# Performance work log

Hardware: AMD Instinct MI355X
Metric: run time of the kernel (lower is better)

## Reference

```python
import jax, jax.numpy as jnp
import numpy as np

B, S, E, H = 2, 2048, 2048, 8
D = E // H          # 256, also PMSNorm width
LAYER_IDX = 3
EPS = 1e-5
NEG = jnp.finfo(jnp.float32).min


def setup_inputs() -> dict:
    key = jax.random.key(0)
    k1, k2, k3 = jax.random.split(key, 3)
    return {
        "hidden_state": jax.random.normal(k1, (B, S, E), dtype=jnp.float32),
        "w_attn": jax.random.normal(k2, (E, 3 * E), dtype=jnp.float32) * 0.02,
        "w_proj": jax.random.normal(k3, (E, E), dtype=jnp.float32) * 0.02,
        "norm_weight": jnp.ones((D,), dtype=jnp.float32),
    }


def reference(hidden_state, w_attn, w_proj, norm_weight):
    # qkv projection (Linear, no bias): [B,S,3E]
    qkv = hidden_state @ w_attn
    q, k, v = jnp.split(qkv, 3, axis=-1)
    # split heads -> [B,H,S,D]
    q = q.reshape(B, S, H, D).transpose(0, 2, 1, 3)
    k = k.reshape(B, S, H, D).transpose(0, 2, 1, 3)
    v = v.reshape(B, S, H, D).transpose(0, 2, 1, 3)
    # scaled scores, extra layer-idx scaling as in the module
    scale = jnp.asarray(D, jnp.float32) ** 0.5 * (LAYER_IDX + 1)
    scores = jnp.einsum("bhqd,bhkd->bhqk", q, k) / scale
    # causal mask (tril buffer): masked positions -> float32 min
    causal = jnp.tril(jnp.ones((S, S), dtype=bool))
    scores = jnp.where(causal[None, None], scores, NEG)
    attn = jax.nn.softmax(scores, axis=-1)  # dropout is identity in eval
    o = jnp.einsum("bhqk,bhkd->bhqd", attn, v)
    # PMSNorm over last dim D (applied per-head, as in the source)
    o = o * jax.lax.rsqrt(jnp.mean(o * o, axis=-1, keepdims=True) + EPS)
    o = o * norm_weight
    # merge heads -> [B,S,E], output projection
    merged = o.transpose(0, 2, 1, 3).reshape(B, S, E)
    return merged @ w_proj
```

## Files before the change

kernel.cpp:

```cpp
#include <hip/hip_runtime.h>
#include <math.h>


typedef unsigned short u16;
typedef unsigned int   u32;
typedef u16   u16x8 __attribute__((ext_vector_type(8)));
typedef __bf16 bf16x8 __attribute__((ext_vector_type(8)));
typedef float f32x4 __attribute__((ext_vector_type(4)));

#define GPTR(p) ((const __attribute__((address_space(1))) void*)(p))
#define LPTR(p) ((__attribute__((address_space(3))) void*)(p))

__device__ __forceinline__ u16 f2bf(float x) {
  u32 u = __float_as_uint(x);
  return (u16)((u + 0x7fffu + ((u >> 16) & 1u)) >> 16);
}

__device__ __forceinline__ bf16x8 ld8(const void* p) {
  u16x8 v = *reinterpret_cast<const u16x8*>(p);
  return __builtin_bit_cast(bf16x8, v);
}

__device__ __forceinline__ void g2l16(const void* g, void* l) {
  __builtin_amdgcn_global_load_lds(GPTR(g), LPTR(l), 16, 0, 0);
}

__global__ void prep_kernel(const float* __restrict__ hs, const float* __restrict__ wat,
                            const float* __restrict__ wpr, u16* __restrict__ Xb,
                            u16* __restrict__ Wa_t, u16* __restrict__ Wp_t) {
  __shared__ float t[32][33];
  const int bid = blockIdx.x, tid = threadIdx.x;
  if (bid < 4096) {
    int i = bid * 256 + tid;
    const float4* p = reinterpret_cast<const float4*>(hs) + (size_t)i * 2;
    float4 a = p[0], b = p[1];
    u16x8 v;
    v[0] = f2bf(a.x); v[1] = f2bf(a.y); v[2] = f2bf(a.z); v[3] = f2bf(a.w);
    v[4] = f2bf(b.x); v[5] = f2bf(b.y); v[6] = f2bf(b.z); v[7] = f2bf(b.w);
    reinterpret_cast<u16x8*>(Xb)[i] = v;
    return;
  }
  const float* in; u16* out; int R, C, bx, by;
  if (bid < 16384) {
    int b2 = bid - 4096;
    in = wat; out = Wa_t; R = 2048; C = 6144;
    bx = (b2 % 192) * 32; by = (b2 / 192) * 32;
  } else {
    int b3 = bid - 16384;
    in = wpr; out = Wp_t; R = 2048; C = 2048;
    bx = (b3 % 64) * 32; by = (b3 / 64) * 32;
  }
  int x = tid & 31, y = tid >> 5;
  #pragma unroll
  for (int k = 0; k < 32; k += 8)
    t[y + k][x] = in[(size_t)(by + y + k) * C + (bx + x)];
  __syncthreads();
  #pragma unroll
  for (int k = 0; k < 32; k += 8)
    out[(size_t)(bx + y + k) * R + (by + x)] = f2bf(t[x][y + k]);
}

__global__ void tv_kernel(const u16* __restrict__ qkv, u16* __restrict__ out) {
  __shared__ u16 t[32][33];
  int bh = blockIdx.z, b = bh >> 3, h = bh & 7;
  const u16* ip = qkv + (size_t)b * 2048 * 6144 + 4096 + h * 256;
  u16* op = out + (size_t)bh * 256 * 2048;
  int bx = blockIdx.x * 32, by = blockIdx.y * 32;
  int x = threadIdx.x, y = threadIdx.y;
  #pragma unroll
  for (int k = 0; k < 32; k += 8)
    t[y + k][x] = ip[(size_t)(by + y + k) * 6144 + (bx + x)];
  __syncthreads();
  #pragma unroll
  for (int k = 0; k < 32; k += 8)
    op[(size_t)(bx + y + k) * 2048 + (by + x)] = t[x][y + k];
}

template<int WM, int WN, int MF, int NF, bool F32OUT>
__global__ __launch_bounds__(512, 4) void gemm2b_kernel(
    const u16* __restrict__ A, const u16* __restrict__ Bt,
    float* __restrict__ Cf, u16* __restrict__ Cb, int M, int N, int K) {
  constexpr int BM = WM * MF * 16;
  constexpr int BN = WN * NF * 16;
  constexpr int TILEB = (BM + BN) * 128;
  constexpr int NSTG = TILEB / 8192;
  __shared__ __align__(16) char smem[2 * TILEB];

  const int tid = threadIdx.x, lane = tid & 63, w = tid >> 6;
  const int wr = w / WN, wc = w % WN;
  const int g = lane >> 4, li = lane & 15;
  const int bn = blockIdx.x * BN, bm = blockIdx.y * BM;

  const char* src[NSTG]; u32 dOff[NSTG];
  #pragma unroll
  for (int j = 0; j < NSTG; ++j) {
    int o = j * 8192 + tid * 16;
    if (o < BM * 128) {
      int row = o >> 7;
      int col = (o & 127) ^ ((row & 7) << 4);
      src[j] = (const char*)A + (size_t)(bm + row) * K * 2 + col;
    } else {
      int rem = o - BM * 128;
      int row = rem >> 7;
      int col = (rem & 127) ^ ((row & 7) << 4);
      src[j] = (const char*)Bt + (size_t)(bn + row) * K * 2 + col;
    }
    dOff[j] = (u32)(o - lane * 16);
  }

  u32 aRd[2][MF], bRd[2][NF];
  #pragma unroll
  for (int ks = 0; ks < 2; ++ks) {
    #pragma unroll
    for (int mf = 0; mf < MF; ++mf) {
      int row = wr * (MF * 16) + mf * 16 + li;
      aRd[ks][mf] = row * 128 + ((ks * 64 + g * 16) ^ ((row & 7) << 4));
    }
    #pragma unroll
    for (int nf = 0; nf < NF; ++nf) {
      int row = wc * (NF * 16) + nf * 16 + li;
      bRd[ks][nf] = BM * 128 + row * 128 + ((ks * 64 + g * 16) ^ ((row & 7) << 4));
    }
  }

  const f32x4 fz = {0.f, 0.f, 0.f, 0.f};
  f32x4 acc[MF][NF];
  #pragma unroll
  for (int i = 0; i < MF; ++i)
    #pragma unroll
    for (int j = 0; j < NF; ++j) acc[i][j] = fz;

  const int NT = K >> 6;
  #pragma unroll
  for (int j = 0; j < NSTG; ++j) { g2l16(src[j], smem + dOff[j]); src[j] += 128; }

  for (int t = 0; t < NT; ++t) {
    const int cur = t & 1;
    const bool more = (t + 1 < NT);
    asm volatile("s_barrier" ::: "memory");
    if (more) {
      char* nb = smem + (cur ^ 1) * TILEB;
      #pragma unroll
      for (int j = 0; j < NSTG; ++j) { g2l16(src[j], nb + dOff[j]); src[j] += 128; }
      asm volatile("s_waitcnt vmcnt(%0)" :: "i"(NSTG) : "memory");
    } else {
      asm volatile("s_waitcnt vmcnt(0)" ::: "memory");
    }
    asm volatile("s_barrier" ::: "memory");

    const char* sb = smem + cur * TILEB;
    #pragma unroll
    for (int ks = 0; ks < 2; ++ks) {
      bf16x8 aR[MF], bR[NF];
      #pragma unroll
      for (int mf = 0; mf < MF; ++mf) aR[mf] = ld8(sb + aRd[ks][mf]);
      #pragma unroll
      for (int nf = 0; nf < NF; ++nf) bR[nf] = ld8(sb + bRd[ks][nf]);
      __builtin_amdgcn_s_setprio(1);
      #pragma unroll
      for (int mf = 0; mf < MF; ++mf)
        #pragma unroll
        for (int nf = 0; nf < NF; ++nf)
          acc[mf][nf] = __builtin_amdgcn_mfma_f32_16x16x32_bf16(aR[mf], bR[nf], acc[mf][nf], 0, 0, 0);
      __builtin_amdgcn_s_setprio(0);
    }
  }

  #pragma unroll
  for (int mf = 0; mf < MF; ++mf)
    #pragma unroll
    for (int nf = 0; nf < NF; ++nf)
      #pragma unroll
      for (int r = 0; r < 4; ++r) {
        int gm = bm + wr * (MF * 16) + mf * 16 + g * 4 + r;
        int gn = bn + wc * (NF * 16) + nf * 16 + li;
        if (F32OUT) Cf[(size_t)gm * N + gn] = acc[mf][nf][r];
        else        Cb[(size_t)gm * N + gn] = f2bf(acc[mf][nf][r]);
      }
}

__global__ __launch_bounds__(512, 2) void attn_kernel(
    const u16* __restrict__ qkv, const u16* __restrict__ Vt,
    const float* __restrict__ nw, u16* __restrict__ Mrg) {
  __shared__ __align__(16) char smem[106496];
  char* sKb = smem;
  char* sVb = smem + 65536;
  char* sPb = smem + 65536 + 32768;
  float* oex  = (float*)smem;
  float* mlex = (float*)(smem + 65536);

  const int c = blockIdx.x;
  const int bh = c & 15, iu = c >> 4;
  const int b = bh >> 3, h = bh & 7;
  const int tid = threadIdx.x, lane = tid & 63, w = tid >> 6;
  const int kh = w >> 2, wq = w & 3;
  const int g = lane >> 4, li = lane & 15;
  const float MASKV = -30000.0f;
  const float MINIT = -1000.0f;
  const float isc = 1.0f / 64.0f;
  const f32x4 fz = {0.f, 0.f, 0.f, 0.f};
  const size_t KADV = (size_t)32 * 6144 * 2;

  #pragma unroll 1
  for (int uu = 0; uu < 2; ++uu) {
    const int qt = uu ? (31 - iu) : iu;
    const int nt = qt + 1;
    const int kvb0 = kh * nt * 32;

    int qrow = qt * 64 + wq * 16 + li;
    const u16* qp = qkv + (size_t)(b * 2048 + qrow) * 6144 + h * 256;
    bf16x8 qf[8];
    #pragma unroll
    for (int c8 = 0; c8 < 8; ++c8) qf[c8] = ld8(qp + c8 * 32 + g * 8);

    const char* kSrc[4]; u32 kDoff[4];
    #pragma unroll
    for (int j = 0; j < 4; ++j) {
      int chunk = wq * 4 + j;
      int o = chunk * 1024 + lane * 16;
      int row = o >> 9, cb = o & 511;
      int cbs = cb ^ ((row & 7) << 4);
      kSrc[j] = (const char*)qkv + ((size_t)(b * 2048 + kvb0 + row) * 6144 + 2048 + h * 256) * 2 + cbs;
      kDoff[j] = chunk * 1024;
    }
    const char* vSrc[4]; char* vDst[4];
    #pragma unroll
    for (int j = 0; j < 4; ++j) {
      int chunk = wq * 4 + j;
      int o = chunk * 1024 + lane * 16;
      int row = o >> 6, cb = o & 63;
      int cbs = cb ^ (((row >> 1) & 3) << 4);
      vSrc[j] = (const char*)Vt + ((size_t)(bh * 256 + row) * 2048 + kvb0) * 2 + cbs;
      vDst[j] = sVb + kh * 16384 + chunk * 1024;
    }

    f32x4 o_[16];
    #pragma unroll
    for (int nf = 0; nf < 16; ++nf) o_[nf] = fz;
    float m_[4] = {MINIT, MINIT, MINIT, MINIT};
    float l_[4] = {0.f, 0.f, 0.f, 0.f};

    {
      char* kb0 = sKb + (kh * 2 + 0) * 16384;
      #pragma unroll
      for (int j = 0; j < 4; ++j) { g2l16(kSrc[j], kb0 + kDoff[j]); kSrc[j] += KADV; }
    }
    asm volatile("s_waitcnt vmcnt(0)" ::: "memory");
    asm volatile("s_barrier" ::: "memory");

    int cur = 0;
    for (int t = 0; t < nt; ++t) {
      const bool more = (t < nt - 1);
      #pragma unroll
      for (int j = 0; j < 4; ++j) { g2l16(vSrc[j], vDst[j]); vSrc[j] += 64; }
      if (more) {
        char* kb = sKb + (kh * 2 + (cur ^ 1)) * 16384;
        #pragma unroll
        for (int j = 0; j < 4; ++j) { g2l16(kSrc[j], kb + kDoff[j]); kSrc[j] += KADV; }
      }

      f32x4 sacc[2];
      const char* kbase = sKb + (kh * 2 + cur) * 16384;
      __builtin_amdgcn_s_setprio(1);
      #pragma unroll
      for (int nf = 0; nf < 2; ++nf) {
        int row = nf * 16 + li;
        int swz = (row & 7) << 4;
        const char* kr = kbase + row * 512;
        f32x4 sa = fz, sb = fz;
        #pragma unroll
        for (int c8 = 0; c8 < 4; ++c8) {
          sa = __builtin_amdgcn_mfma_f32_16x16x32_bf16(qf[c8],     ld8(kr + ((c8 * 64 + g * 16) ^ swz)),       sa, 0, 0, 0);
          sb = __builtin_amdgcn_mfma_f32_16x16x32_bf16(qf[c8 + 4], ld8(kr + (((c8 + 4) * 64 + g * 16) ^ swz)), sb, 0, 0, 0);
        }
        sacc[nf] = sa + sb;
      }
      __builtin_amdgcn_s_setprio(0);

      const int tidx = kh * nt + t;
      const bool diag = (tidx >= 2 * qt);
      float p[2][4], m0[4];
      #pragma unroll
      for (int r = 0; r < 4; ++r) {
        int qr = qt * 64 + wq * 16 + g * 4 + r;
        float a0 = sacc[0][r] * isc;
        float a1 = sacc[1][r] * isc;
        if (diag) {
          if (tidx * 32 + li > qr) a0 = MASKV;
          if (tidx * 32 + 16 + li > qr) a1 = MASKV;
        }
        p[0][r] = a0; p[1][r] = a1;
        m0[r] = fmaxf(a0, a1);
      }
      bool need = (m0[0] > m_[0] + 8.f) || (m0[1] > m_[1] + 8.f) ||
                  (m0[2] > m_[2] + 8.f) || (m0[3] > m_[3] + 8.f);
      if (__any(need)) {
        #pragma unroll
        for (int r = 0; r < 4; ++r) {
          float mx = m0[r];
          mx = fmaxf(mx, __shfl_xor(mx, 1));
          mx = fmaxf(mx, __shfl_xor(mx, 2));
          mx = fmaxf(mx, __shfl_xor(mx, 4));
          mx = fmaxf(mx, __shfl_xor(mx, 8));
          float mn = fmaxf(m_[r], mx);
          float sc = __expf(m_[r] - mn);
          l_[r] *= sc; m_[r] = mn;
          #pragma unroll
          for (int nf = 0; nf < 16; ++nf) o_[nf][r] *= sc;
        }
      }
      #pragma unroll
      for (int r = 0; r < 4; ++r) {
        float e0 = __expf(p[0][r] - m_[r]);
        float e1 = __expf(p[1][r] - m_[r]);
        p[0][r] = e0; p[1][r] = e1;
        l_[r] += e0 + e1;
      }

      if (more) asm volatile("s_waitcnt vmcnt(4)" ::: "memory");
      else      asm volatile("s_waitcnt vmcnt(0)" ::: "memory");
      asm volatile("s_barrier" ::: "memory");

      char* sPw = sPb + kh * 4096 + wq * 1024;
      #pragma unroll
      for (int r = 0; r < 4; ++r) {
        int row = g * 4 + r;
        int swz = ((row >> 1) & 3) << 4;
        #pragma unroll
        for (int nf = 0; nf < 2; ++nf)
          *(u16*)(sPw + row * 64 + (((nf * 16 + li) * 2) ^ swz)) = f2bf(p[nf][r]);
      }
      asm volatile("s_waitcnt lgkmcnt(0)" ::: "memory");
      __builtin_amdgcn_sched_barrier(0);

      __builtin_amdgcn_s_setprio(1);
      {
        const char* vb = sVb + kh * 16384;
        bf16x8 pa = ld8(sPw + li * 64 + ((g * 16) ^ (((li >> 1) & 3) << 4)));
        #pragma unroll
        for (int nf = 0; nf < 16; ++nf) {
          int row = nf * 16 + li;
          bf16x8 vf = ld8(vb + row * 64 + ((g * 16) ^ (((row >> 1) & 3) << 4)));
          o_[nf] = __builtin_amdgcn_mfma_f32_16x16x32_bf16(pa, vf, o_[nf], 0, 0, 0);
        }
      }
      __builtin_amdgcn_s_setprio(0);

      asm volatile("s_barrier" ::: "memory");
      if (more) asm volatile("s_waitcnt vmcnt(0)" ::: "memory");
      cur ^= 1;
    }

    if (kh == 1) {
      #pragma unroll
      for (int nf = 0; nf < 16; ++nf)
        *(f32x4*)(oex + wq * 4096 + nf * 256 + lane * 4) = o_[nf];
      #pragma unroll
      for (int r = 0; r < 4; ++r) {
        mlex[wq * 512 + r * 64 + lane] = l_[r];
        mlex[wq * 512 + 256 + r * 64 + lane] = m_[r];
      }
    }
    __syncthreads();
    if (kh == 0) {
      float aw[4], bw[4], inv_l[4];
      #pragma unroll
      for (int r = 0; r < 4; ++r) {
        float mB = mlex[wq * 512 + 256 + r * 64 + lane];
        float lB = mlex[wq * 512 + r * 64 + lane];
        float mm = fmaxf(m_[r], mB);
        aw[r] = __expf(m_[r] - mm);
        bw[r] = __expf(mB - mm);
        float lr = l_[r] * aw[r] + lB * bw[r];
        lr += __shfl_xor(lr, 1);
        lr += __shfl_xor(lr, 2);
        lr += __shfl_xor(lr, 4);
        lr += __shfl_xor(lr, 8);
        inv_l[r] = 1.0f / lr;
      }
      #pragma unroll
      for (int nf = 0; nf < 16; ++nf) {
        f32x4 ob = *(f32x4*)(oex + wq * 4096 + nf * 256 + lane * 4);
        #pragma unroll
        for (int r = 0; r < 4; ++r)
          o_[nf][r] = o_[nf][r] * aw[r] + ob[r] * bw[r];
      }
      #pragma unroll
      for (int r = 0; r < 4; ++r) {
        float ss = 0.f;
        #pragma unroll
        for (int nf = 0; nf < 16; ++nf) {
          float v = o_[nf][r] * inv_l[r];
          ss += v * v;
        }
        ss += __shfl_xor(ss, 1);
        ss += __shfl_xor(ss, 2);
        ss += __shfl_xor(ss, 4);
        ss += __shfl_xor(ss, 8);
        float rms = rsqrtf(ss * (1.0f / 256.0f) + 1e-5f);
        int row = qt * 64 + wq * 16 + g * 4 + r;
        #pragma unroll
        for (int nf = 0; nf < 16; ++nf) {
          int d = nf * 16 + li;
          float v = o_[nf][r] * inv_l[r] * rms * nw[d];
          Mrg[((size_t)(b * 2048 + row)) * 2048 + h * 256 + d] = f2bf(v);
        }
      }
    }
    __syncthreads();
  }
}

extern "C" void kernel_launch(void* const* d_in, const int* in_sizes, int n_in,
                              void* d_out, int out_size, void* d_ws, size_t ws_size,
                              hipStream_t stream) {
  const float* hs  = (const float*)d_in[0];
  const float* wat = (const float*)d_in[1];
  const float* wpr = (const float*)d_in[2];
  const float* nw  = (const float*)d_in[3];
  float* out = (float*)d_out;

  char* ws = (char*)d_ws;
  u16* Xb   = (u16*)(ws + 0);
  u16* Wp_t = (u16*)(ws + (16u << 20));
  u16* Qkv  = (u16*)(ws + (24u << 20));
  u16* Vt   = (u16*)(ws + (72u << 20));
  u16* Mrg  = Xb;
  u16* Wa_t = (u16*)d_out;

  dim3 t328(32, 8);
  prep_kernel<<<20480, 256, 0, stream>>>(hs, wat, wpr, Xb, Wa_t, Wp_t);
  gemm2b_kernel<2, 4, 4, 3, false><<<dim3(32, 32), 512, 0, stream>>>(
      Xb, Wa_t, nullptr, Qkv, 4096, 6144, 2048);
  tv_kernel<<<dim3(8, 64, 16), t328, 0, stream>>>(Qkv, Vt);
  attn_kernel<<<256, 512, 0, stream>>>(Qkv, Vt, nw, Mrg);
  gemm2b_kernel<2, 4, 4, 2, true><<<dim3(16, 32), 512, 0, stream>>>(
      Mrg, Wp_t, out, nullptr, 4096, 2048, 2048);
  (void)in_sizes; (void)n_in; (void)out_size; (void)ws_size;
}
```

Measured before the change: 233.1 us.

## Split attention KV halves into separate blocks with a merge kernel

The in-block split-K attention, where two warp groups each handled half of the KV range and merged through shared memory, becomes a split-KV scheme across separate 256-thread blocks. Each block writes a normalized bf16 partial output and its log-sum-exp to global memory. A new merge kernel combines the two partials and applies the RMS norm. This doubles the grid and cuts shared memory per block, which should improve occupancy and scheduling, at the cost of an extra launch, a global round trip for the partials, and bf16 rounding of the partial outputs.

```diff
diff --git a/kernel.cpp b/kernel.cpp
--- a/kernel.cpp
+++ b/kernel.cpp
@@ -14,6 +14,10 @@
 __device__ __forceinline__ u16 f2bf(float x) {
   u32 u = __float_as_uint(x);
   return (u16)((u + 0x7fffu + ((u >> 16) & 1u)) >> 16);
+}
+
+__device__ __forceinline__ float bf2f(u16 x) {
+  return __uint_as_float(((u32)x) << 16);
 }
 
 __device__ __forceinline__ bf16x8 ld8(const void* p) {
@@ -179,21 +183,17 @@
       }
 }
 
-__global__ __launch_bounds__(512, 2) void attn_kernel(
+__global__ __launch_bounds__(256, 2) void attn_main_kernel(
     const u16* __restrict__ qkv, const u16* __restrict__ Vt,
-    const float* __restrict__ nw, u16* __restrict__ Mrg) {
-  __shared__ __align__(16) char smem[106496];
-  char* sKb = smem;
-  char* sVb = smem + 65536;
-  char* sPb = smem + 65536 + 32768;
-  float* oex  = (float*)smem;
-  float* mlex = (float*)(smem + 65536);
+    u16* __restrict__ Opart, float* __restrict__ Lse) {
+  __shared__ __align__(16) u16 sK[2][32 * 256];
+  __shared__ __align__(16) u16 sV[256 * 32];
+  __shared__ __align__(16) u16 sP[4 * 16 * 32];
 
   const int c = blockIdx.x;
-  const int bh = c & 15, iu = c >> 4;
+  const int bh = c & 15, iu = (c >> 4) & 15, half = c >> 8;
   const int b = bh >> 3, h = bh & 7;
-  const int tid = threadIdx.x, lane = tid & 63, w = tid >> 6;
-  const int kh = w >> 2, wq = w & 3;
+  const int tid = threadIdx.x, lane = tid & 63, wq = tid >> 6;
   const int g = lane >> 4, li = lane & 15;
   const float MASKV = -30000.0f;
   const float MINIT = -1000.0f;
@@ -205,7 +205,7 @@
   for (int uu = 0; uu < 2; ++uu) {
     const int qt = uu ? (31 - iu) : iu;
     const int nt = qt + 1;
-    const int kvb0 = kh * nt * 32;
+    const int kvb0 = half * nt * 32;
 
     int qrow = qt * 64 + wq * 16 + li;
     const u16* qp = qkv + (size_t)(b * 2048 + qrow) * 6144 + h * 256;
@@ -231,7 +231,7 @@
       int row = o >> 6, cb = o & 63;
       int cbs = cb ^ (((row >> 1) & 3) << 4);
       vSrc[j] = (const char*)Vt + ((size_t)(bh * 256 + row) * 2048 + kvb0) * 2 + cbs;
-      vDst[j] = sVb + kh * 16384 + chunk * 1024;
+      vDst[j] = (char*)sV + chunk * 1024;
     }
 
     f32x4 o_[16];
@@ -240,11 +240,8 @@
     float m_[4] = {MINIT, MINIT, MINIT, MINIT};
     float l_[4] = {0.f, 0.f, 0.f, 0.f};
 
-    {
-      char* kb0 = sKb + (kh * 2 + 0) * 16384;
-      #pragma unroll
-      for (int j = 0; j < 4; ++j) { g2l16(kSrc[j], kb0 + kDoff[j]); kSrc[j] += KADV; }
-    }
+    #pragma unroll
+    for (int j = 0; j < 4; ++j) { g2l16(kSrc[j], (char*)sK[0] + kDoff[j]); kSrc[j] += KADV; }
     asm volatile("s_waitcnt vmcnt(0)" ::: "memory");
     asm volatile("s_barrier" ::: "memory");
 
@@ -254,13 +251,13 @@
       #pragma unroll
       for (int j = 0; j < 4; ++j) { g2l16(vSrc[j], vDst[j]); vSrc[j] += 64; }
       if (more) {
-        char* kb = sKb + (kh * 2 + (cur ^ 1)) * 16384;
+        char* kb = (char*)sK[cur ^ 1];
         #pragma unroll
         for (int j = 0; j < 4; ++j) { g2l16(kSrc[j], kb + kDoff[j]); kSrc[j] += KADV; }
       }
 
       f32x4 sacc[2];
-      const char* kbase = sKb + (kh * 2 + cur) * 16384;
+      const char* kbase = (const char*)sK[cur];
       __builtin_amdgcn_s_setprio(1);
       #pragma unroll
       for (int nf = 0; nf < 2; ++nf) {
@@ -277,7 +274,7 @@
       }
       __builtin_amdgcn_s_setprio(0);
 
-      const int tidx = kh * nt + t;
+      const int tidx = half * nt + t;
       const bool diag = (tidx >= 2 * qt);
       float p[2][4], m0[4];
       #pragma unroll
@@ -321,7 +318,7 @@
       else      asm volatile("s_waitcnt vmcnt(0)" ::: "memory");
       asm volatile("s_barrier" ::: "memory");
 
-      char* sPw = sPb + kh * 4096 + wq * 1024;
+      char* sPw = (char*)sP + wq * 1024;
       #pragma unroll
       for (int r = 0; r < 4; ++r) {
         int row = g * 4 + r;
@@ -335,12 +332,11 @@
 
       __builtin_amdgcn_s_setprio(1);
       {
-        const char* vb = sVb + kh * 16384;
         bf16x8 pa = ld8(sPw + li * 64 + ((g * 16) ^ (((li >> 1) & 3) << 4)));
         #pragma unroll
         for (int nf = 0; nf < 16; ++nf) {
           int row = nf * 16 + li;
-          bf16x8 vf = ld8(vb + row * 64 + ((g * 16) ^ (((row >> 1) & 3) << 4)));
+          bf16x8 vf = ld8((const char*)sV + row * 64 + ((g * 16) ^ (((row >> 1) & 3) << 4)));
           o_[nf] = __builtin_amdgcn_mfma_f32_16x16x32_bf16(pa, vf, o_[nf], 0, 0, 0);
         }
       }
@@ -351,63 +347,70 @@
       cur ^= 1;
     }
 
-    if (kh == 1) {
+    const int pu = (bh * 32 + qt) * 2 + half;
+    u16* op = Opart + (size_t)pu * 16384;
+    #pragma unroll
+    for (int r = 0; r < 4; ++r) {
+      float ls = l_[r];
+      ls += __shfl_xor(ls, 1);
+      ls += __shfl_xor(ls, 2);
+      ls += __shfl_xor(ls, 4);
+      ls += __shfl_xor(ls, 8);
+      float linv = (ls > 0.f) ? 1.0f / ls : 0.f;
+      float lse  = (ls > 0.f) ? (m_[r] + __logf(ls)) : -3.0e38f;
+      int rloc = wq * 16 + g * 4 + r;
+      if (li == 0) Lse[pu * 64 + rloc] = lse;
       #pragma unroll
       for (int nf = 0; nf < 16; ++nf)
-        *(f32x4*)(oex + wq * 4096 + nf * 256 + lane * 4) = o_[nf];
-      #pragma unroll
-      for (int r = 0; r < 4; ++r) {
-        mlex[wq * 512 + r * 64 + lane] = l_[r];
-        mlex[wq * 512 + 256 + r * 64 + lane] = m_[r];
-      }
+        op[rloc * 256 + nf * 16 + li] = f2bf(o_[nf][r] * linv);
     }
     __syncthreads();
-    if (kh == 0) {
-      float aw[4], bw[4], inv_l[4];
-      #pragma unroll
-      for (int r = 0; r < 4; ++r) {
-        float mB = mlex[wq * 512 + 256 + r * 64 + lane];
-        float lB = mlex[wq * 512 + r * 64 + lane];
-        float mm = fmaxf(m_[r], mB);
-        aw[r] = __expf(m_[r] - mm);
-        bw[r] = __expf(mB - mm);
-        float lr = l_[r] * aw[r] + lB * bw[r];
-        lr += __shfl_xor(lr, 1);
-        lr += __shfl_xor(lr, 2);
-        lr += __shfl_xor(lr, 4);
-        lr += __shfl_xor(lr, 8);
-        inv_l[r] = 1.0f / lr;
-      }
-      #pragma unroll
-      for (int nf = 0; nf < 16; ++nf) {
-        f32x4 ob = *(f32x4*)(oex + wq * 4096 + nf * 256 + lane * 4);
-        #pragma unroll
-        for (int r = 0; r < 4; ++r)
-          o_[nf][r] = o_[nf][r] * aw[r] + ob[r] * bw[r];
-      }
-      #pragma unroll
-      for (int r = 0; r < 4; ++r) {
-        float ss = 0.f;
-        #pragma unroll
-        for (int nf = 0; nf < 16; ++nf) {
-          float v = o_[nf][r] * inv_l[r];
-          ss += v * v;
-        }
-        ss += __shfl_xor(ss, 1);
-        ss += __shfl_xor(ss, 2);
-        ss += __shfl_xor(ss, 4);
-        ss += __shfl_xor(ss, 8);
-        float rms = rsqrtf(ss * (1.0f / 256.0f) + 1e-5f);
-        int row = qt * 64 + wq * 16 + g * 4 + r;
-        #pragma unroll
-        for (int nf = 0; nf < 16; ++nf) {
-          int d = nf * 16 + li;
-          float v = o_[nf][r] * inv_l[r] * rms * nw[d];
-          Mrg[((size_t)(b * 2048 + row)) * 2048 + h * 256 + d] = f2bf(v);
-        }
-      }
-    }
-    __syncthreads();
+  }
+}
+
+__global__ __launch_bounds__(256) void attn_merge_kernel(
+    const u16* __restrict__ Opart, const float* __restrict__ Lse,
+    const float* __restrict__ nw, u16* __restrict__ Mrg) {
+  const int c = blockIdx.x;
+  const int bh = c >> 5, qt = c & 31;
+  const int b = bh >> 3, h = bh & 7;
+  const int tid = threadIdx.x;
+  const int rloc = tid >> 2, dg = tid & 3;
+
+  const int puA = (bh * 32 + qt) * 2, puB = puA + 1;
+  float mA = Lse[puA * 64 + rloc], mB = Lse[puB * 64 + rloc];
+  float M = fmaxf(mA, mB);
+  float wA = __expf(mA - M), wB = __expf(mB - M);
+  float dnm = wA + wB;
+  wA /= dnm; wB /= dnm;
+
+  const u16* pA = Opart + (size_t)puA * 16384 + rloc * 256 + dg * 64;
+  const u16* pB = Opart + (size_t)puB * 16384 + rloc * 256 + dg * 64;
+  float ov[64];
+  float ss = 0.f;
+  #pragma unroll
+  for (int j = 0; j < 8; ++j) {
+    u16x8 a = *reinterpret_cast<const u16x8*>(pA + j * 8);
+    u16x8 bb = *reinterpret_cast<const u16x8*>(pB + j * 8);
+    #pragma unroll
+    for (int e = 0; e < 8; ++e) {
+      float o = wA * bf2f(a[e]) + wB * bf2f(bb[e]);
+      ov[j * 8 + e] = o;
+      ss += o * o;
+    }
+  }
+  ss += __shfl_xor(ss, 1);
+  ss += __shfl_xor(ss, 2);
+  float rms = rsqrtf(ss * (1.0f / 256.0f) + 1e-5f);
+
+  u16* mp = Mrg + ((size_t)(b * 2048 + qt * 64 + rloc)) * 2048 + h * 256 + dg * 64;
+  #pragma unroll
+  for (int j = 0; j < 8; ++j) {
+    u16x8 v;
+    #pragma unroll
+    for (int e = 0; e < 8; ++e)
+      v[e] = f2bf(ov[j * 8 + e] * rms * nw[dg * 64 + j * 8 + e]);
+    *reinterpret_cast<u16x8*>(mp + j * 8) = v;
   }
 }
 
@@ -421,19 +424,22 @@
   float* out = (float*)d_out;
 
   char* ws = (char*)d_ws;
-  u16* Xb   = (u16*)(ws + 0);
-  u16* Wp_t = (u16*)(ws + (16u << 20));
-  u16* Qkv  = (u16*)(ws + (24u << 20));
-  u16* Vt   = (u16*)(ws + (72u << 20));
-  u16* Mrg  = Xb;
-  u16* Wa_t = (u16*)d_out;
+  u16* Xb    = (u16*)(ws + 0);
+  u16* Wp_t  = (u16*)(ws + (16u << 20));
+  u16* Qkv   = (u16*)(ws + (24u << 20));
+  u16* Vt    = (u16*)(ws + (72u << 20));
+  u16* Mrg   = Vt;
+  float* Lse = (float*)Xb;
+  u16* Wa_t  = (u16*)d_out;
+  u16* Opart = (u16*)d_out;
 
   dim3 t328(32, 8);
   prep_kernel<<<20480, 256, 0, stream>>>(hs, wat, wpr, Xb, Wa_t, Wp_t);
   gemm2b_kernel<2, 4, 4, 3, false><<<dim3(32, 32), 512, 0, stream>>>(
       Xb, Wa_t, nullptr, Qkv, 4096, 6144, 2048);
   tv_kernel<<<dim3(8, 64, 16), t328, 0, stream>>>(Qkv, Vt);
-  attn_kernel<<<256, 512, 0, stream>>>(Qkv, Vt, nw, Mrg);
+  attn_main_kernel<<<512, 256, 0, stream>>>(Qkv, Vt, Opart, Lse);
+  attn_merge_kernel<<<512, 256, 0, stream>>>(Opart, Lse, nw, Mrg);
   gemm2b_kernel<2, 4, 4, 2, true><<<dim3(16, 32), 512, 0, stream>>>(
       Mrg, Wp_t, out, nullptr, 4096, 2048, 2048);
   (void)in_sizes; (void)n_in; (void)out_size; (void)ws_size;
```

Measured after the change: 250.9 us. 1.08x slower.
